# Kernel tuning notes

Measured on AMD Instinct MI355X. Metric: run time of the kernel, lower is better.

Reference implementation:

```python
import jax, jax.numpy as jnp
import numpy as np

NBINS = 256


def _equalize_hist(img):
    # img: [H, W] float32 with values in [0, 255]; replicates cv2.equalizeHist
    vals = jnp.clip(img.astype(jnp.int32), 0, NBINS - 1).reshape(-1)
    hist = jnp.zeros((NBINS,), jnp.float32).at[vals].add(1.0)
    cdf = jnp.cumsum(hist)
    total = jnp.float32(vals.shape[0])
    # cdf value at the first nonzero bin (cv2 maps that bin to 0)
    cdf_min = cdf[jnp.argmax(hist > 0)]
    scale = (NBINS - 1.0) / jnp.maximum(total - cdf_min, 1.0)
    lut = jnp.clip(jnp.round((cdf - cdf_min) * scale), 0.0, 255.0)
    return lut[vals].reshape(img.shape) / 255.0


def setup_inputs() -> dict:
    key = jax.random.key(0)
    k1, _ = jax.random.split(key)
    # uint8-like pixel values stored as float32, shape [B, 1, H, W]
    image = jnp.floor(jax.random.uniform(k1, (64, 1, 1024, 1024), jnp.float32) * 256.0)
    image = jnp.clip(image, 0.0, 255.0)
    kernel = jnp.array([[[[0.0, 1.0, 0.0], [1.0, -4.0, 1.0], [0.0, 1.0, 0.0]]]], jnp.float32)
    return {"image": image, "kernel": kernel}


def reference(image, kernel):
    # per-image histogram equalization (channels == 1, as in the torch loop)
    eq = jax.vmap(_equalize_hist)(image[:, 0, :, :])[:, None, :, :]  # [B,1,H,W]
    laplace = jax.lax.conv_general_dilated(
        eq, kernel,
        window_strides=(1, 1), padding=((1, 1), (1, 1)),
        dimension_numbers=("NCHW", "OIHW", "NCHW"))
    # torch.var defaults to unbiased (ddof=1) over all elements
    return jnp.var(laplace, ddof=1)
```

## Files before the change

kernel.cpp:

```cpp
#include <hip/hip_runtime.h>

#define W 1024
#define H 1024
#define NIMG 64
#define NBINS 256
#define NPIX (W * H)
#define NTOT ((long long)NIMG * NPIX)
#define NSLOT 256
#define RSTRIP 16

typedef float f32x4 __attribute__((ext_vector_type(4)));

#define WS_HIST 0
#define WS_LUTP 65536
#define WS_ACC  81920
#define WS_SMALL 86016
#define WS_U8   (128 * 1024)
#define WS_FAST (WS_U8 + (size_t)NIMG * NPIX)

__device__ __forceinline__ int lut_gather(unsigned int lutw, int v) {
    unsigned int w = (unsigned int)__builtin_amdgcn_ds_bpermute(v & 0xFC, (int)lutw);
    return (int)((w >> ((v & 3) << 3)) & 0xFFu);
}

template <bool WRITE_U8>
__global__ __launch_bounds__(256) void hist_kernel(const float* __restrict__ img,
                                                   unsigned int* __restrict__ ghist,
                                                   unsigned char* __restrict__ u8img) {
    __shared__ unsigned int lh[NBINS];
    const int b = blockIdx.y;
    lh[threadIdx.x] = 0u;
    __syncthreads();
    const size_t base = (size_t)b * NPIX;
    const f32x4* p = (const f32x4*)(img + base);
    uchar4* q8 = (uchar4*)(u8img + base);
    const int nvec = NPIX / 4;
    const int stride = gridDim.x * 256;
    for (int i = blockIdx.x * 256 + threadIdx.x; i < nvec; i += stride) {
        f32x4 v = WRITE_U8 ? __builtin_nontemporal_load(&p[i]) : p[i];
        int i0 = min(max((int)v[0], 0), 255);
        int i1 = min(max((int)v[1], 0), 255);
        int i2 = min(max((int)v[2], 0), 255);
        int i3 = min(max((int)v[3], 0), 255);
        atomicAdd(&lh[i0], 1u);
        atomicAdd(&lh[i1], 1u);
        atomicAdd(&lh[i2], 1u);
        atomicAdd(&lh[i3], 1u);
        if (WRITE_U8) {
            q8[i] = make_uchar4((unsigned char)i0, (unsigned char)i1,
                                (unsigned char)i2, (unsigned char)i3);
        }
    }
    __syncthreads();
    unsigned int c = lh[threadIdx.x];
    if (c) atomicAdd(&ghist[b * NBINS + threadIdx.x], c);
}

__global__ __launch_bounds__(256) void lut_kernel(const unsigned int* __restrict__ ghist,
                                                  unsigned int* __restrict__ lutp) {
    __shared__ float cdf[NBINS];
    __shared__ unsigned char lut8[NBINS];
    __shared__ float s_min;
    const int b = blockIdx.x;
    const int t = threadIdx.x;
    cdf[t] = (float)ghist[b * NBINS + t];
    __syncthreads();
    for (int off = 1; off < NBINS; off <<= 1) {
        float add = (t >= off) ? cdf[t - off] : 0.0f;
        __syncthreads();
        cdf[t] += add;
        __syncthreads();
    }
    if (t == 0) {
        float m = 0.0f;
        for (int i = 0; i < NBINS; ++i) {
            if (cdf[i] > 0.0f) { m = cdf[i]; break; }
        }
        s_min = m;
    }
    __syncthreads();
    const float scale = 255.0f / fmaxf((float)NPIX - s_min, 1.0f);
    float L = fminf(fmaxf(rintf((cdf[t] - s_min) * scale), 0.0f), 255.0f);
    lut8[t] = (unsigned char)L;
    __syncthreads();
    if (t < 64) {
        unsigned int w = (unsigned int)lut8[4 * t] |
                         ((unsigned int)lut8[4 * t + 1] << 8) |
                         ((unsigned int)lut8[4 * t + 2] << 16) |
                         ((unsigned int)lut8[4 * t + 3] << 24);
        lutp[b * 64 + t] = w;
    }
}

template <bool USE_U8>
__global__ __launch_bounds__(256) void lap_kernel(const float* __restrict__ img,
                                                  const unsigned char* __restrict__ u8img,
                                                  const unsigned int* __restrict__ lutp,
                                                  unsigned long long* __restrict__ acc) {
    __shared__ unsigned short eqS[RSTRIP + 2][W];
    const int b = blockIdx.y;
    const int y0 = blockIdx.x * RSTRIP;
    const int t = threadIdx.x;
    const int x0 = t * 4;
    const unsigned int lutw = lutp[b * 64 + (t & 63)];
    const size_t base = (size_t)b * NPIX;

    for (int r = 0; r < RSTRIP + 2; ++r) {
        const int gy = y0 - 1 + r;
        ushort4 e = make_ushort4(0, 0, 0, 0);
        if (gy >= 0 && gy < H) {
            int v0, v1, v2, v3;
            if (USE_U8) {
                uchar4 c = *(const uchar4*)(u8img + base + (size_t)gy * W + x0);
                v0 = c.x; v1 = c.y; v2 = c.z; v3 = c.w;
            } else {
                f32x4 c = *(const f32x4*)(img + base + (size_t)gy * W + x0);
                v0 = min(max((int)c[0], 0), 255);
                v1 = min(max((int)c[1], 0), 255);
                v2 = min(max((int)c[2], 0), 255);
                v3 = min(max((int)c[3], 0), 255);
            }
            e.x = (unsigned short)lut_gather(lutw, v0);
            e.y = (unsigned short)lut_gather(lutw, v1);
            e.z = (unsigned short)lut_gather(lutw, v2);
            e.w = (unsigned short)lut_gather(lutw, v3);
        }
        *(ushort4*)&eqS[r][x0] = e;
    }
    __syncthreads();

    int s = 0;
    int q = 0;
    for (int r = 1; r <= RSTRIP; ++r) {
        ushort4 c = *(const ushort4*)&eqS[r][x0];
        ushort4 u = *(const ushort4*)&eqS[r - 1][x0];
        ushort4 d = *(const ushort4*)&eqS[r + 1][x0];
        const int el = (x0 > 0) ? (int)eqS[r][x0 - 1] : 0;
        const int er = (x0 + 4 < W) ? (int)eqS[r][x0 + 4] : 0;
        const int c0 = c.x, c1 = c.y, c2 = c.z, c3 = c.w;
        const int l0 = (int)u.x + (int)d.x + el + c1 - 4 * c0;
        const int l1 = (int)u.y + (int)d.y + c0 + c2 - 4 * c1;
        const int l2 = (int)u.z + (int)d.z + c1 + c3 - 4 * c2;
        const int l3 = (int)u.w + (int)d.w + c2 + er - 4 * c3;
        s += l0 + l1 + l2 + l3;
        q += __mul24(l0, l0) + __mul24(l1, l1) + __mul24(l2, l2) + __mul24(l3, l3);
    }

    long long S = s, Q = q;
    for (int off = 32; off > 0; off >>= 1) {
        S += __shfl_down(S, off, 64);
        Q += __shfl_down(Q, off, 64);
    }
    __shared__ long long ss[4], sq[4];
    const int wave = t >> 6, lane = t & 63;
    if (lane == 0) { ss[wave] = S; sq[wave] = Q; }
    __syncthreads();
    if (t == 0) {
        long long St = ss[0] + ss[1] + ss[2] + ss[3];
        long long Qt = sq[0] + sq[1] + sq[2] + sq[3];
        const int slot = (blockIdx.x + blockIdx.y * gridDim.x) & (NSLOT - 1);
        atomicAdd(&acc[2 * slot], (unsigned long long)St);
        atomicAdd(&acc[2 * slot + 1], (unsigned long long)Qt);
    }
}

__global__ __launch_bounds__(256) void finalize_kernel(const unsigned long long* __restrict__ acc,
                                                       float* __restrict__ out) {
    const int t = threadIdx.x;
    long long S = (long long)acc[2 * t];
    long long Q = (long long)acc[2 * t + 1];
    for (int off = 32; off > 0; off >>= 1) {
        S += __shfl_down(S, off, 64);
        Q += __shfl_down(Q, off, 64);
    }
    __shared__ long long ss[4], sq[4];
    const int wave = t >> 6, lane = t & 63;
    if (lane == 0) { ss[wave] = S; sq[wave] = Q; }
    __syncthreads();
    if (t == 0) {
        long long St = ss[0] + ss[1] + ss[2] + ss[3];
        long long Qt = sq[0] + sq[1] + sq[2] + sq[3];
        const double N = (double)NTOT;
        double Sr = (double)St / 255.0;
        double Qr = (double)Qt / 65025.0;
        out[0] = (float)((Qr - Sr * Sr / N) / (N - 1.0));
    }
}

extern "C" void kernel_launch(void* const* d_in, const int* in_sizes, int n_in,
                              void* d_out, int out_size, void* d_ws, size_t ws_size,
                              hipStream_t stream) {
    const float* img = (const float*)d_in[0];
    float* out = (float*)d_out;

    unsigned int* ghist       = (unsigned int*)((char*)d_ws + WS_HIST);
    unsigned int* lutp        = (unsigned int*)((char*)d_ws + WS_LUTP);
    unsigned long long* acc   = (unsigned long long*)((char*)d_ws + WS_ACC);
    unsigned char* u8img      = (unsigned char*)((char*)d_ws + WS_U8);

    const bool fast = (ws_size >= WS_FAST);

    hipMemsetAsync(d_ws, 0, WS_SMALL, stream);

    dim3 hgrid(64, NIMG);
    if (fast) hist_kernel<true><<<hgrid, 256, 0, stream>>>(img, ghist, u8img);
    else      hist_kernel<false><<<hgrid, 256, 0, stream>>>(img, ghist, u8img);

    lut_kernel<<<NIMG, NBINS, 0, stream>>>(ghist, lutp);

    dim3 lgrid(H / RSTRIP, NIMG);
    if (fast) lap_kernel<true><<<lgrid, 256, 0, stream>>>(img, u8img, lutp, acc);
    else      lap_kernel<false><<<lgrid, 256, 0, stream>>>(img, u8img, lutp, acc);

    finalize_kernel<<<1, 256, 0, stream>>>(acc, out);
}
```

Baseline: 136.9 us.

## Restructure Laplacian kernel to register-rolling rows per wave without shared memory

The Laplacian kernel drops its shared-memory strip. Each wave now owns 8 consecutive rows and each lane handles 16 columns, with packed 8-bit equalized values held in registers as a rolling three-row window. Horizontal neighbours come from lane shuffles, and the next row is prefetched while the current one is computed. Per-block LDS staging and the barrier go away, and each wave does its own atomic into the slot accumulator. The trade is more bpermute gathers per lane, more register pressure, and more global atomics. A second change makes the histogram pass always use nontemporal loads.

Measured after the change: 127.1 us. 1.08x faster.

```diff
diff --git a/kernel.cpp b/kernel.cpp
--- a/kernel.cpp
+++ b/kernel.cpp
@@ -7,7 +7,7 @@
 #define NPIX (W * H)
 #define NTOT ((long long)NIMG * NPIX)
 #define NSLOT 256
-#define RSTRIP 16
+#define RPW 8
 
 typedef float f32x4 __attribute__((ext_vector_type(4)));
 
@@ -17,11 +17,6 @@
 #define WS_SMALL 86016
 #define WS_U8   (128 * 1024)
 #define WS_FAST (WS_U8 + (size_t)NIMG * NPIX)
-
-__device__ __forceinline__ int lut_gather(unsigned int lutw, int v) {
-    unsigned int w = (unsigned int)__builtin_amdgcn_ds_bpermute(v & 0xFC, (int)lutw);
-    return (int)((w >> ((v & 3) << 3)) & 0xFFu);
-}
 
 template <bool WRITE_U8>
 __global__ __launch_bounds__(256) void hist_kernel(const float* __restrict__ img,
@@ -37,7 +32,7 @@
     const int nvec = NPIX / 4;
     const int stride = gridDim.x * 256;
     for (int i = blockIdx.x * 256 + threadIdx.x; i < nvec; i += stride) {
-        f32x4 v = WRITE_U8 ? __builtin_nontemporal_load(&p[i]) : p[i];
+        f32x4 v = __builtin_nontemporal_load(&p[i]);
         int i0 = min(max((int)v[0], 0), 255);
         int i1 = min(max((int)v[1], 0), 255);
         int i2 = min(max((int)v[2], 0), 255);
@@ -97,53 +92,88 @@
                                                   const unsigned char* __restrict__ u8img,
                                                   const unsigned int* __restrict__ lutp,
                                                   unsigned long long* __restrict__ acc) {
-    __shared__ unsigned short eqS[RSTRIP + 2][W];
     const int b = blockIdx.y;
-    const int y0 = blockIdx.x * RSTRIP;
-    const int t = threadIdx.x;
-    const int x0 = t * 4;
-    const unsigned int lutw = lutp[b * 64 + (t & 63)];
+    const int lane = threadIdx.x & 63;
+    const int wv = threadIdx.x >> 6;
+    const int y0 = blockIdx.x * (RPW * 4) + wv * RPW;
+    const int col0 = lane * 16;
+    const unsigned int lutw = lutp[b * 64 + lane];
     const size_t base = (size_t)b * NPIX;
-
-    for (int r = 0; r < RSTRIP + 2; ++r) {
-        const int gy = y0 - 1 + r;
-        ushort4 e = make_ushort4(0, 0, 0, 0);
-        if (gy >= 0 && gy < H) {
-            int v0, v1, v2, v3;
+    const unsigned char* rowp8 = u8img + base + col0;
+    const float* rowpf = img + base + col0;
+
+    unsigned int p_[4], c_[4], n_[4];
+
+    auto load_raw = [&](int gy, unsigned int raw[4]) {
+        if ((unsigned)gy < (unsigned)H) {
             if (USE_U8) {
-                uchar4 c = *(const uchar4*)(u8img + base + (size_t)gy * W + x0);
-                v0 = c.x; v1 = c.y; v2 = c.z; v3 = c.w;
+                uint4 r = *(const uint4*)(rowp8 + (size_t)gy * W);
+                raw[0] = r.x; raw[1] = r.y; raw[2] = r.z; raw[3] = r.w;
             } else {
-                f32x4 c = *(const f32x4*)(img + base + (size_t)gy * W + x0);
-                v0 = min(max((int)c[0], 0), 255);
-                v1 = min(max((int)c[1], 0), 255);
-                v2 = min(max((int)c[2], 0), 255);
-                v3 = min(max((int)c[3], 0), 255);
+                const f32x4* fp = (const f32x4*)(rowpf + (size_t)gy * W);
+#pragma unroll
+                for (int k = 0; k < 4; ++k) {
+                    f32x4 v = fp[k];
+                    unsigned int w = (unsigned int)min(max((int)v[0], 0), 255);
+                    w |= (unsigned int)min(max((int)v[1], 0), 255) << 8;
+                    w |= (unsigned int)min(max((int)v[2], 0), 255) << 16;
+                    w |= (unsigned int)min(max((int)v[3], 0), 255) << 24;
+                    raw[k] = w;
+                }
             }
-            e.x = (unsigned short)lut_gather(lutw, v0);
-            e.y = (unsigned short)lut_gather(lutw, v1);
-            e.z = (unsigned short)lut_gather(lutw, v2);
-            e.w = (unsigned short)lut_gather(lutw, v3);
-        }
-        *(ushort4*)&eqS[r][x0] = e;
-    }
-    __syncthreads();
-
-    int s = 0;
-    int q = 0;
-    for (int r = 1; r <= RSTRIP; ++r) {
-        ushort4 c = *(const ushort4*)&eqS[r][x0];
-        ushort4 u = *(const ushort4*)&eqS[r - 1][x0];
-        ushort4 d = *(const ushort4*)&eqS[r + 1][x0];
-        const int el = (x0 > 0) ? (int)eqS[r][x0 - 1] : 0;
-        const int er = (x0 + 4 < W) ? (int)eqS[r][x0 + 4] : 0;
-        const int c0 = c.x, c1 = c.y, c2 = c.z, c3 = c.w;
-        const int l0 = (int)u.x + (int)d.x + el + c1 - 4 * c0;
-        const int l1 = (int)u.y + (int)d.y + c0 + c2 - 4 * c1;
-        const int l2 = (int)u.z + (int)d.z + c1 + c3 - 4 * c2;
-        const int l3 = (int)u.w + (int)d.w + c2 + er - 4 * c3;
-        s += l0 + l1 + l2 + l3;
-        q += __mul24(l0, l0) + __mul24(l1, l1) + __mul24(l2, l2) + __mul24(l3, l3);
+        } else {
+            raw[0] = raw[1] = raw[2] = raw[3] = 0u;
+        }
+    };
+    auto gather_row = [&](const unsigned int raw[4], bool valid, unsigned int ew[4]) {
+#pragma unroll
+        for (int k = 0; k < 4; ++k) {
+            unsigned int out = 0u;
+#pragma unroll
+            for (int j = 0; j < 4; ++j) {
+                int v = (int)((raw[k] >> (8 * j)) & 0xFFu);
+                unsigned int e = (unsigned int)__builtin_amdgcn_ds_bpermute(v & 0xFC, (int)lutw);
+                out |= ((e >> ((v & 3) << 3)) & 0xFFu) << (8 * j);
+            }
+            ew[k] = valid ? out : 0u;
+        }
+    };
+
+    unsigned int rawB[4], rawC[4];
+    load_raw(y0 - 1, rawB);
+    gather_row(rawB, y0 - 1 >= 0, p_);
+    load_raw(y0, rawB);
+    gather_row(rawB, true, c_);
+    load_raw(y0 + 1, rawB);
+
+    int s = 0, q = 0;
+#pragma unroll
+    for (int rr = 0; rr < RPW; ++rr) {
+        const int gy = y0 + rr;
+        if (rr + 1 < RPW) load_raw(gy + 2, rawC);
+        gather_row(rawB, gy + 1 < H, n_);
+
+        unsigned int t3 = (unsigned int)__shfl_up((int)c_[3], 1, 64);
+        const int lw = (lane == 0) ? 0 : (int)(t3 >> 24);
+        unsigned int t0 = (unsigned int)__shfl_down((int)c_[0], 1, 64);
+        const int rw = (lane == 63) ? 0 : (int)(t0 & 0xFFu);
+
+#pragma unroll
+        for (int p = 0; p < 16; ++p) {
+            const int k = p >> 2, sh = (p & 3) << 3;
+            const int c = (int)((c_[k] >> sh) & 0xFFu);
+            const int u = (int)((p_[k] >> sh) & 0xFFu);
+            const int d = (int)((n_[k] >> sh) & 0xFFu);
+            const int l = (p == 0) ? lw
+                        : (int)((c_[(p - 1) >> 2] >> (((p - 1) & 3) << 3)) & 0xFFu);
+            const int r = (p == 15) ? rw
+                        : (int)((c_[(p + 1) >> 2] >> (((p + 1) & 3) << 3)) & 0xFFu);
+            const int lap = u + d + l + r - 4 * c;
+            s += lap;
+            q += lap * lap;
+        }
+#pragma unroll
+        for (int k = 0; k < 4; ++k) { p_[k] = c_[k]; c_[k] = n_[k]; rawB[k] = rawC[k]; }
     }
 
     long long S = s, Q = q;
@@ -151,16 +181,11 @@
         S += __shfl_down(S, off, 64);
         Q += __shfl_down(Q, off, 64);
     }
-    __shared__ long long ss[4], sq[4];
-    const int wave = t >> 6, lane = t & 63;
-    if (lane == 0) { ss[wave] = S; sq[wave] = Q; }
-    __syncthreads();
-    if (t == 0) {
-        long long St = ss[0] + ss[1] + ss[2] + ss[3];
-        long long Qt = sq[0] + sq[1] + sq[2] + sq[3];
-        const int slot = (blockIdx.x + blockIdx.y * gridDim.x) & (NSLOT - 1);
-        atomicAdd(&acc[2 * slot], (unsigned long long)St);
-        atomicAdd(&acc[2 * slot + 1], (unsigned long long)Qt);
+    if (lane == 0) {
+        const int wid = (blockIdx.x + blockIdx.y * gridDim.x) * 4 + wv;
+        const int slot = wid & (NSLOT - 1);
+        atomicAdd(&acc[2 * slot], (unsigned long long)S);
+        atomicAdd(&acc[2 * slot + 1], (unsigned long long)Q);
     }
 }
 
@@ -193,10 +218,10 @@
     const float* img = (const float*)d_in[0];
     float* out = (float*)d_out;
 
-    unsigned int* ghist       = (unsigned int*)((char*)d_ws + WS_HIST);
-    unsigned int* lutp        = (unsigned int*)((char*)d_ws + WS_LUTP);
-    unsigned long long* acc   = (unsigned long long*)((char*)d_ws + WS_ACC);
-    unsigned char* u8img      = (unsigned char*)((char*)d_ws + WS_U8);
+    unsigned int* ghist     = (unsigned int*)((char*)d_ws + WS_HIST);
+    unsigned int* lutp      = (unsigned int*)((char*)d_ws + WS_LUTP);
+    unsigned long long* acc = (unsigned long long*)((char*)d_ws + WS_ACC);
+    unsigned char* u8img    = (unsigned char*)((char*)d_ws + WS_U8);
 
     const bool fast = (ws_size >= WS_FAST);
 
@@ -208,7 +233,7 @@
 
     lut_kernel<<<NIMG, NBINS, 0, stream>>>(ghist, lutp);
 
-    dim3 lgrid(H / RSTRIP, NIMG);
+    dim3 lgrid(H / (RPW * 4), NIMG);
     if (fast) lap_kernel<true><<<lgrid, 256, 0, stream>>>(img, u8img, lutp, acc);
     else      lap_kernel<false><<<lgrid, 256, 0, stream>>>(img, u8img, lutp, acc);
 
```
